# Performance work log

Measured on AMD Instinct MI355X. Metric: run time of the kernel, lower is better.

## Reference

```python
import jax, jax.numpy as jnp
import numpy as np
from jax import lax

EPS = 1e-5

def _conv(x, w, b, pad):
    y = lax.conv_general_dilated(x, w, (1, 1), [(pad, pad), (pad, pad)],
                                 dimension_numbers=('NCHW', 'OIHW', 'NCHW'))
    return y + b[None, :, None, None]

def _bn(x, g, b, m, v):
    # eval-mode BatchNorm2d with running stats
    scale = g * lax.rsqrt(v + EPS)
    return x * scale[None, :, None, None] + (b - m * scale)[None, :, None, None]

def setup_inputs() -> dict:
    key = jax.random.key(0)
    ks = jax.random.split(key, 16)
    B, C, H, W = 16, 64, 128, 128
    C2 = 2 * C
    d = {}
    d['x'] = jax.random.normal(ks[0], (B, C, H, W), jnp.float32)
    # fc1: Conv2d(C,C,3,p=1) + BN(C)
    d['fc1_w'] = jax.random.normal(ks[1], (C, C, 3, 3), jnp.float32) * 0.05
    d['fc1_b'] = jax.random.normal(ks[2], (C,), jnp.float32) * 0.05
    d['bn1_g'] = jnp.ones((C,), jnp.float32)
    d['bn1_b'] = jnp.zeros((C,), jnp.float32)
    d['bn1_m'] = jax.random.normal(ks[3], (C,), jnp.float32) * 0.05
    d['bn1_v'] = jax.random.uniform(ks[4], (C,), jnp.float32) * 0.5 + 0.5
    # graph_conv.nn: Conv2d(2C,2C,1) + BN(2C) + GELU
    d['gc_w'] = jax.random.normal(ks[5], (C2, C2, 1, 1), jnp.float32) * 0.05
    d['gc_b'] = jax.random.normal(ks[6], (C2,), jnp.float32) * 0.05
    d['bng_g'] = jnp.ones((C2,), jnp.float32)
    d['bng_b'] = jnp.zeros((C2,), jnp.float32)
    d['bng_m'] = jax.random.normal(ks[7], (C2,), jnp.float32) * 0.05
    d['bng_v'] = jax.random.uniform(ks[8], (C2,), jnp.float32) * 0.5 + 0.5
    # fc2: Conv2d(2C,C,3,p=1) + BN(C)
    d['fc2_w'] = jax.random.normal(ks[9], (C, C2, 3, 3), jnp.float32) * 0.05
    d['fc2_b'] = jax.random.normal(ks[10], (C,), jnp.float32) * 0.05
    d['bn2_g'] = jnp.ones((C,), jnp.float32)
    d['bn2_b'] = jnp.zeros((C,), jnp.float32)
    d['bn2_m'] = jax.random.normal(ks[11], (C,), jnp.float32) * 0.05
    d['bn2_v'] = jax.random.uniform(ks[12], (C,), jnp.float32) * 0.5 + 0.5
    return d

def reference(x, fc1_w, fc1_b, bn1_g, bn1_b, bn1_m, bn1_v,
              gc_w, gc_b, bng_g, bng_b, bng_m, bng_v,
              fc2_w, fc2_b, bn2_g, bn2_b, bn2_m, bn2_v):
    # fc1
    h = _bn(_conv(x, fc1_w, fc1_b, 1), bn1_g, bn1_b, bn1_m, bn1_v)
    # MRConv4dSP: strided self-attention over superpatch tokens
    sel = h[:, :, ::4, ::4]                          # [B,C,h4,w4]
    B, C, h4, w4 = sel.shape
    q = sel.reshape(B, C, h4 * w4).transpose(0, 2, 1)  # [B,N,C]
    scale = C ** (-0.5)
    att = jax.nn.softmax(jnp.einsum('bnc,bmc->bnm', q, q) * scale, axis=-1)
    o = jnp.einsum('bnm,bmc->bnc', att, q)           # [B,N,C]
    o = o.transpose(0, 2, 1).reshape(B, C, h4, w4)
    o = jnp.repeat(jnp.repeat(o, 4, axis=2), 4, axis=3)
    g = jnp.concatenate([h, o], axis=1)              # [B,2C,H,W]
    g = jax.nn.gelu(_bn(_conv(g, gc_w, gc_b, 0), bng_g, bng_b, bng_m, bng_v),
                    approximate=False)
    # fc2 + residual (drop_path=0 -> identity)
    y = _bn(_conv(g, fc2_w, fc2_b, 1), bn2_g, bn2_b, bn2_m, bn2_v)
    return y + x
```

## Files before the change

### kernel.cpp

```cpp
#include <hip/hip_runtime.h>
#include <math.h>

#define EPSV 1e-5f

typedef __bf16 bf16;
using bf16x8 = __attribute__((ext_vector_type(8))) __bf16;
using bf16x4 = __attribute__((ext_vector_type(4))) __bf16;
using bf16x2 = __attribute__((ext_vector_type(2))) __bf16;
using f32x4  = __attribute__((ext_vector_type(4))) float;

static __device__ __forceinline__ f32x4 mfma16(bf16x8 a, bf16x8 b, f32x4 c) {
    return __builtin_amdgcn_mfma_f32_16x16x32_bf16(a, b, c, 0, 0, 0);
}
static __device__ __forceinline__ f32x4 zero4() {
    f32x4 z = {0.f, 0.f, 0.f, 0.f};
    return z;
}

typedef __attribute__((address_space(1))) const char g_char_t;
typedef __attribute__((address_space(3))) char lds_char_t;
static __device__ __forceinline__ void gll16(const void* g, void* l) {
    __builtin_amdgcn_global_load_lds((g_char_t*)g, (lds_char_t*)l, 16, 0, 0);
}

static __device__ __forceinline__ float gelu_f(float v) {
    float z = fabsf(v) * 0.70710678118f;
    float t = __builtin_amdgcn_rcpf(1.f + 0.3275911f * z);
    float poly = t * (0.254829592f + t * (-0.284496736f + t * (1.421413741f +
                 t * (-1.453152027f + t * 1.061405429f))));
    float e = __expf(-z * z);
    float erfv = copysignf(1.f - poly * e, v);
    return 0.5f * v * (1.f + erfv);
}

template<int CIN>
__global__ __launch_bounds__(256) void prep_conv_w(const float* __restrict__ w,
                                                   bf16* __restrict__ wt)
{
    int t = blockIdx.x * 256 + threadIdx.x;
    if (t >= 64 * CIN) return;
    int cout = t / CIN, ci = t - cout * CIN;
    int cci = ci >> 5, lg = (ci >> 3) & 3, j = ci & 7;
    int mi = cout >> 4, lix = cout & 15;
#pragma unroll
    for (int kgt = 0; kgt < 9; ++kgt) {
        float v = w[(size_t)t * 9 + kgt];
        wt[((((size_t)kgt * (CIN >> 5) + cci) * 4 + mi) * 64 + lg * 16 + lix) * 8 + j]
            = (bf16)v;
    }
}

__global__ __launch_bounds__(256) void prep_1x1_w(const float* __restrict__ w,
                                                  bf16* __restrict__ wt)
{
    int t = blockIdx.x * 256 + threadIdx.x;
    int cout = t >> 7, ci = t & 127;
    int ks = ci >> 5, lg = (ci >> 3) & 3, j = ci & 7;
    wt[(((size_t)(ks * 4 + lg) * 128) + cout) * 8 + j] = (bf16)w[t];
}

__global__ __launch_bounds__(256) void cvt_x_nhwc(const float* __restrict__ x,
                                                  bf16* __restrict__ xb,
                                                  float* __restrict__ zb)
{
    __shared__ float t_lds[64 * 68];
    const int bx = blockIdx.x;
    const int b  = blockIdx.y;
    const int y  = bx >> 1, x0 = (bx & 1) * 64;
    const int tid = threadIdx.x;

    if (bx == 0 && b == 0 && tid < 64)
        ((float4*)zb)[tid] = make_float4(0.f, 0.f, 0.f, 0.f);

    for (int f = tid; f < 64 * 16; f += 256) {
        int c = f >> 4, xu = f & 15;
        float4 v = *(const float4*)&x[((size_t)(b * 64 + c) << 14) + (y << 7) + x0 + xu * 4];
        t_lds[(xu * 4 + 0) * 68 + c] = v.x;
        t_lds[(xu * 4 + 1) * 68 + c] = v.y;
        t_lds[(xu * 4 + 2) * 68 + c] = v.z;
        t_lds[(xu * 4 + 3) * 68 + c] = v.w;
    }
    __syncthreads();
    for (int f = tid; f < 64 * 8; f += 256) {
        int xx = f >> 3, cu = f & 7;
        const float* p = &t_lds[xx * 68 + cu * 8];
        bf16x8 v;
#pragma unroll
        for (int j = 0; j < 8; ++j) v[j] = (bf16)p[j];
        *(bf16x8*)&xb[((size_t)((b * 128 + y) * 128) + x0 + xx) * 64 + cu * 8] = v;
    }
}

template<int CIN, int OUTMODE>
__global__ __launch_bounds__(512) void conv3x3_mfma(
    const bf16* __restrict__ in, const bf16* __restrict__ wt,
    const float* __restrict__ bias,
    const float* __restrict__ bg, const float* __restrict__ bb,
    const float* __restrict__ bm, const float* __restrict__ bv,
    const bf16* __restrict__ resid, const bf16* __restrict__ zb,
    void* __restrict__ outp)
{
    constexpr int NC = CIN >> 5;
    __shared__ bf16 in_lds[672 * 32];
    __shared__ bf16 w_lds[36 * 512];

    const int wg = blockIdx.x;
    const int v  = (wg & 7) * 64 + (wg >> 3);
    const int tile = v & 31, b = v >> 5;
    const int x0 = (tile & 1) * 64;
    const int y0 = (tile >> 1) * 8;
    const int tid  = threadIdx.x;
    const int wid  = tid >> 6;
    const int lane = tid & 63;
    const int lix  = lane & 15, lg = lane >> 4;

    int goff[6]; bool gok[6];
#pragma unroll
    for (int i = 0; i < 6; ++i) {
        int chunk = wid + 8 * i;
        int f = chunk * 64 + lane;
        int pix = f >> 2, u = f & 3;
        int iy = pix / 66, ix = pix - iy * 66;
        int gy = y0 + iy - 1, gx = x0 + ix - 1;
        gok[i]  = (chunk < 42) && (pix < 660) &&
                  (unsigned)gy < 128u && (unsigned)gx < 128u;
        goff[i] = ((b * 128 + gy) * 128 + gx) * CIN + u * 8;
    }
    int rd[9];
#pragma unroll
    for (int kg = 0; kg < 3; ++kg)
#pragma unroll
        for (int t = 0; t < 3; ++t)
            rd[kg * 3 + t] = ((wid + kg) * 66 + lix + t) * 32 + lg * 8;

    f32x4 acc[4][4];
#pragma unroll
    for (int i = 0; i < 4; ++i)
#pragma unroll
        for (int j = 0; j < 4; ++j) acc[i][j] = zero4();

    auto issue_in = [&](int cci) {
#pragma unroll
        for (int i = 0; i < 6; ++i) {
            int chunk = wid + 8 * i;
            if (chunk < 42) {
                const void* src = gok[i] ? (const void*)(in + goff[i] + cci * 32)
                                         : (const void*)zb;
                gll16(src, (char*)in_lds + chunk * 1024);
            }
        }
    };
    auto issue_w = [&](int cci) {
#pragma unroll
        for (int i = 0; i < 5; ++i) {
            int chunk = wid + 8 * i;
            if (chunk < 36) {
                const bf16* src = wt + ((size_t)(chunk >> 2) * NC + cci) * 2048
                                     + (chunk & 3) * 512 + lane * 8;
                gll16(src, (char*)w_lds + chunk * 1024);
            }
        }
    };
    auto compute = [&]() {
#pragma unroll
        for (int kgt = 0; kgt < 9; ++kgt) {
            bf16x8 af[4];
#pragma unroll
            for (int mi = 0; mi < 4; ++mi)
                af[mi] = *(const bf16x8*)&w_lds[(kgt * 4 + mi) * 512 + lane * 8];
#pragma unroll
            for (int nj = 0; nj < 4; ++nj) {
                bf16x8 bfr = *(const bf16x8*)&in_lds[rd[kgt] + nj * 512];
#pragma unroll
                for (int mi = 0; mi < 4; ++mi)
                    acc[mi][nj] = mfma16(af[mi], bfr, acc[mi][nj]);
            }
        }
    };

    issue_in(0);
    issue_w(0);
#pragma unroll 1
    for (int c = 0; c < NC; ++c) {
        asm volatile("s_waitcnt vmcnt(0)" ::: "memory");
        __syncthreads();
        compute();
        if (c + 1 < NC) {
            __syncthreads();
            issue_in(c + 1);
            issue_w(c + 1);
        }
    }

    if (OUTMODE == 0) {
        bf16* out = (bf16*)outp;
        bf16* stg = in_lds;
#pragma unroll 1
        for (int p = 0; p < 2; ++p) {
            __syncthreads();
            if ((wid >> 2) == p) {
                int rl = wid & 3;
#pragma unroll
                for (int mi = 0; mi < 4; ++mi) {
                    float A[4], Bc[4];
#pragma unroll
                    for (int r = 0; r < 4; ++r) {
                        int c = mi * 16 + lg * 4 + r;
                        float s = bg[c] * rsqrtf(bv[c] + EPSV);
                        A[r]  = s;
                        Bc[r] = bias[c] * s + bb[c] - bm[c] * s;
                    }
#pragma unroll
                    for (int nj = 0; nj < 4; ++nj) {
                        int px = nj * 16 + lix;
                        bf16x4 vv;
#pragma unroll
                        for (int r = 0; r < 4; ++r)
                            vv[r] = (bf16)(acc[mi][nj][r] * A[r] + Bc[r]);
                        *(bf16x4*)&stg[(rl * 64 + px) * 68 + mi * 16 + lg * 4] = vv;
                    }
                }
            }
            __syncthreads();
#pragma unroll
            for (int k = 0; k < 4; ++k) {
                int idx = k * 512 + tid;
                int row = idx >> 9, rem = idx & 511;
                int px = rem >> 3, cu = rem & 7;
                bf16x8 vv = *(const bf16x8*)&stg[(row * 64 + px) * 68 + cu * 8];
                *(bf16x8*)&out[((size_t)((b * 128 + y0 + p * 4 + row) * 128)
                                + x0 + px) * 64 + cu * 8] = vv;
            }
        }
    } else {
        float* out = (float*)outp;
        const int gy = y0 + wid;
#pragma unroll
        for (int mi = 0; mi < 4; ++mi) {
            float A[4], Bc[4];
#pragma unroll
            for (int r = 0; r < 4; ++r) {
                int c = mi * 16 + lg * 4 + r;
                float s = bg[c] * rsqrtf(bv[c] + EPSV);
                A[r]  = s;
                Bc[r] = bias[c] * s + bb[c] - bm[c] * s;
            }
#pragma unroll
            for (int nj = 0; nj < 4; ++nj) {
                int px = x0 + nj * 16 + lix;
                bf16x4 rv = *(const bf16x4*)&resid[((size_t)((b * 128 + gy) * 128) + px) * 64
                                                   + mi * 16 + lg * 4];
#pragma unroll
                for (int r = 0; r < 4; ++r) {
                    int c = mi * 16 + lg * 4 + r;
                    size_t oi = ((size_t)(b * 64 + c) << 14) + (gy << 7) + px;
                    out[oi] = acc[mi][nj][r] * A[r] + Bc[r] + (float)rv[r];
                }
            }
        }
    }
}

__global__ __launch_bounds__(256) void gather_q(const bf16* __restrict__ h,
                                                bf16* __restrict__ q)
{
    int t = blockIdx.x * 256 + threadIdx.x;
    int cu = t & 7, n = (t >> 3) & 1023, b = t >> 13;
    int y = (n >> 5) << 2, x = (n & 31) << 2;
    bf16x8 v = *(const bf16x8*)&h[((size_t)((b * 128 + y) * 128 + x)) * 64 + cu * 8];
    *(bf16x8*)&q[((size_t)(b * 1024 + n)) * 64 + cu * 8] = v;
}

__global__ __launch_bounds__(256) void attn_fused(const bf16* __restrict__ q,
                                                  bf16* __restrict__ o)
{
    __shared__ bf16 qn[64 * 72];
    __shared__ bf16 kn[128 * 72];
    __shared__ bf16 vt[64 * 136];
    __shared__ bf16 pl[4][16 * 136];
    __shared__ __align__(16) float fac[4][16];
    const int n0 = blockIdx.x * 64, b = blockIdx.y;
    const int tid = threadIdx.x, w = tid >> 6, lane = tid & 63;
    const int lix = lane & 15, lg = lane >> 4;
    const bf16* qb = q + ((size_t)b << 16);

    for (int f = tid; f < 512; f += 256) {
        int row = f >> 3, cu = f & 7;
        *(bf16x8*)&qn[row * 72 + cu * 8] =
            *(const bf16x8*)&qb[(size_t)(n0 + row) * 64 + cu * 8];
    }

    float m_run = -3.0e38f, l_run = 0.f;
    f32x4 oacc[4];
#pragma unroll
    for (int ct = 0; ct < 4; ++ct) oacc[ct] = zero4();

    for (int mt = 0; mt < 1024; mt += 128) {
        __syncthreads();
        for (int f = tid; f < 1024; f += 256) {
            int row = f >> 3, cu = f & 7;
            *(bf16x8*)&kn[row * 72 + cu * 8] =
                *(const bf16x8*)&qb[(size_t)(mt + row) * 64 + cu * 8];
        }
        for (int f = tid; f < 512; f += 256) {
            int mp = f >> 3, cu = f & 7;
            int m = mp * 2;
            bf16x8 a = *(const bf16x8*)&qb[(size_t)(mt + m) * 64 + cu * 8];
            bf16x8 c = *(const bf16x8*)&qb[(size_t)(mt + m + 1) * 64 + cu * 8];
#pragma unroll
            for (int j = 0; j < 8; ++j) {
                bf16x2 pr = {a[j], c[j]};
                *(bf16x2*)&vt[(cu * 8 + j) * 136 + m] = pr;
            }
        }
        __syncthreads();

        bf16x8 bq0 = *(const bf16x8*)&qn[(w * 16 + lix) * 72 + lg * 8];
        bf16x8 bq1 = *(const bf16x8*)&qn[(w * 16 + lix) * 72 + 32 + lg * 8];

        f32x4 s[8];
#pragma unroll
        for (int t = 0; t < 8; ++t) {
            bf16x8 a0 = *(const bf16x8*)&kn[(t * 16 + lix) * 72 + lg * 8];
            bf16x8 a1 = *(const bf16x8*)&kn[(t * 16 + lix) * 72 + 32 + lg * 8];
            s[t] = mfma16(a0, bq0, zero4());
            s[t] = mfma16(a1, bq1, s[t]);
        }

        float mx = -3.0e38f;
#pragma unroll
        for (int t = 0; t < 8; ++t)
#pragma unroll
            for (int r = 0; r < 4; ++r) { s[t][r] *= 0.125f; mx = fmaxf(mx, s[t][r]); }
        mx = fmaxf(mx, __shfl_xor(mx, 16));
        mx = fmaxf(mx, __shfl_xor(mx, 32));
        float m_new = fmaxf(m_run, mx);
        float alpha = __expf(m_run - m_new);

        float psum = 0.f;
#pragma unroll
        for (int t = 0; t < 8; ++t) {
            float p0 = __expf(s[t][0] - m_new), p1 = __expf(s[t][1] - m_new);
            float p2 = __expf(s[t][2] - m_new), p3 = __expf(s[t][3] - m_new);
            psum += (p0 + p1) + (p2 + p3);
            bf16x2 v01 = {(bf16)p0, (bf16)p1};
            bf16x2 v23 = {(bf16)p2, (bf16)p3};
            *(bf16x2*)&pl[w][lix * 136 + t * 16 + lg * 4]     = v01;
            *(bf16x2*)&pl[w][lix * 136 + t * 16 + lg * 4 + 2] = v23;
        }
        psum += __shfl_xor(psum, 16);
        psum += __shfl_xor(psum, 32);
        l_run = l_run * alpha + psum;
        m_run = m_new;
        if (lg == 0) fac[w][lix] = alpha;

        float4 a4 = *(const float4*)&fac[w][lg * 4];
        float aa[4] = {a4.x, a4.y, a4.z, a4.w};
#pragma unroll
        for (int ct = 0; ct < 4; ++ct)
#pragma unroll
            for (int r = 0; r < 4; ++r) oacc[ct][r] *= aa[r];

#pragma unroll
        for (int kk = 0; kk < 4; ++kk) {
            bf16x8 pa = *(const bf16x8*)&pl[w][lix * 136 + kk * 32 + lg * 8];
#pragma unroll
            for (int ct = 0; ct < 4; ++ct) {
                bf16x8 bv = *(const bf16x8*)&vt[(ct * 16 + lix) * 136 + kk * 32 + lg * 8];
                oacc[ct] = mfma16(pa, bv, oacc[ct]);
            }
        }
    }

    if (lg == 0) fac[w][lix] = l_run;
    float4 l4 = *(const float4*)&fac[w][lg * 4];
    float ll[4] = {1.f / l4.x, 1.f / l4.y, 1.f / l4.z, 1.f / l4.w};
#pragma unroll
    for (int ct = 0; ct < 4; ++ct)
#pragma unroll
        for (int r = 0; r < 4; ++r) {
            int n = n0 + w * 16 + lg * 4 + r;
            int c = ct * 16 + lix;
            o[((size_t)(b * 1024 + n)) * 64 + c] = (bf16)(oacc[ct][r] * ll[r]);
        }
}

__global__ __launch_bounds__(256) void conv1x1_mfma(
    const bf16* __restrict__ h, const bf16* __restrict__ ov,
    const bf16* __restrict__ wt, const float* __restrict__ bias,
    const float* __restrict__ bg, const float* __restrict__ bb,
    const float* __restrict__ bm, const float* __restrict__ bv,
    bf16* __restrict__ g)
{
    __shared__ bf16 in1[128 * 136];
    const int y = blockIdx.x, b = blockIdx.y;
    const int tid = threadIdx.x;
    const int wid = tid >> 6, lane = tid & 63;
    const int lix = lane & 15, lg = lane >> 4;
    const int wm = wid >> 1, wn = wid & 1;

    for (int f = tid; f < 128 * 16; f += 256) {
        int px = f >> 4, cu = f & 15;
        bf16x8 v;
        if (cu < 8) {
            v = *(const bf16x8*)&h[((size_t)((b * 128 + y) * 128 + px)) * 64 + cu * 8];
        } else {
            int n = ((y >> 2) << 5) + (px >> 2);
            v = *(const bf16x8*)&ov[((size_t)(b * 1024 + n)) * 64 + (cu - 8) * 8];
        }
        *(bf16x8*)&in1[px * 136 + cu * 8] = v;
    }
    __syncthreads();

    f32x4 acc[4][4];
#pragma unroll
    for (int i = 0; i < 4; ++i)
#pragma unroll
        for (int j = 0; j < 4; ++j) acc[i][j] = zero4();

#pragma unroll
    for (int ks = 0; ks < 4; ++ks) {
        bf16x8 af[4], bfv[4];
#pragma unroll
        for (int mi = 0; mi < 4; ++mi)
            af[mi] = *(const bf16x8*)&wt[(((size_t)(ks * 4 + lg) * 128) + wm * 64 + mi * 16 + lix) * 8];
#pragma unroll
        for (int nj = 0; nj < 4; ++nj)
            bfv[nj] = *(const bf16x8*)&in1[(wn * 64 + nj * 16 + lix) * 136 + ks * 32 + lg * 8];
#pragma unroll
        for (int mi = 0; mi < 4; ++mi)
#pragma unroll
            for (int nj = 0; nj < 4; ++nj)
                acc[mi][nj] = mfma16(af[mi], bfv[nj], acc[mi][nj]);
    }

    __syncthreads();
    bf16* stg = in1;
#pragma unroll
    for (int mi = 0; mi < 4; ++mi) {
        float A[4], Bc[4];
#pragma unroll
        for (int r = 0; r < 4; ++r) {
            int c = wm * 64 + mi * 16 + lg * 4 + r;
            float s = bg[c] * rsqrtf(bv[c] + EPSV);
            A[r]  = s;
            Bc[r] = bias[c] * s + bb[c] - bm[c] * s;
        }
#pragma unroll
        for (int nj = 0; nj < 4; ++nj) {
            int px = wn * 64 + nj * 16 + lix;
            bf16x4 vv;
#pragma unroll
            for (int r = 0; r < 4; ++r)
                vv[r] = (bf16)gelu_f(acc[mi][nj][r] * A[r] + Bc[r]);
            *(bf16x4*)&stg[px * 132 + wm * 64 + mi * 16 + lg * 4] = vv;
        }
    }
    __syncthreads();
#pragma unroll
    for (int k = 0; k < 8; ++k) {
        int idx = k * 256 + tid;
        int px = idx >> 4, cu = idx & 15;
        bf16x8 v = *(const bf16x8*)&stg[px * 132 + cu * 8];
        *(bf16x8*)&g[((size_t)((b * 128 + y) * 128) + px) * 128 + cu * 8] = v;
    }
}

extern "C" void kernel_launch(void* const* d_in, const int* in_sizes, int n_in,
                              void* d_out, int out_size, void* d_ws, size_t ws_size,
                              hipStream_t stream)
{
    const float* x     = (const float*)d_in[0];
    const float* fc1_w = (const float*)d_in[1];
    const float* fc1_b = (const float*)d_in[2];
    const float* bn1_g = (const float*)d_in[3];
    const float* bn1_b = (const float*)d_in[4];
    const float* bn1_m = (const float*)d_in[5];
    const float* bn1_v = (const float*)d_in[6];
    const float* gc_w  = (const float*)d_in[7];
    const float* gc_b  = (const float*)d_in[8];
    const float* bng_g = (const float*)d_in[9];
    const float* bng_b = (const float*)d_in[10];
    const float* bng_m = (const float*)d_in[11];
    const float* bng_v = (const float*)d_in[12];
    const float* fc2_w = (const float*)d_in[13];
    const float* fc2_b = (const float*)d_in[14];
    const float* bn2_g = (const float*)d_in[15];
    const float* bn2_b = (const float*)d_in[16];
    const float* bn2_m = (const float*)d_in[17];
    const float* bn2_v = (const float*)d_in[18];

    char* wsb = (char*)d_ws;
    bf16* x_bf = (bf16*)wsb;
    bf16* h    = (bf16*)(wsb + 33554432);
    bf16* g    = (bf16*)(wsb + 67108864);
    bf16* q    = (bf16*)(wsb + 134217728);
    bf16* o    = (bf16*)(wsb + 136314880);
    bf16* wt1  = (bf16*)(wsb + 138412032);
    bf16* wt2  = (bf16*)(wsb + 138485760);
    bf16* wtg  = (bf16*)(wsb + 138633216);
    bf16* zb   = (bf16*)(wsb + 138665984);

    prep_conv_w<64><<<16, 256, 0, stream>>>(fc1_w, wt1);
    prep_conv_w<128><<<32, 256, 0, stream>>>(fc2_w, wt2);
    prep_1x1_w<<<64, 256, 0, stream>>>(gc_w, wtg);

    cvt_x_nhwc<<<dim3(256, 16), 256, 0, stream>>>(x, x_bf, (float*)zb);

    conv3x3_mfma<64, 0><<<512, 512, 0, stream>>>(
        x_bf, wt1, fc1_b, bn1_g, bn1_b, bn1_m, bn1_v, nullptr, zb, h);

    gather_q<<<512, 256, 0, stream>>>(h, q);

    attn_fused<<<dim3(16, 16), 256, 0, stream>>>(q, o);

    conv1x1_mfma<<<dim3(128, 16), 256, 0, stream>>>(
        h, o, wtg, gc_b, bng_g, bng_b, bng_m, bng_v, g);

    conv3x3_mfma<128, 1><<<512, 512, 0, stream>>>(
        g, wt2, fc2_b, bn2_g, bn2_b, bn2_m, bn2_v, x_bf, zb, (float*)d_out);
}
```

Measured before the change: 189.2 us.

## Double-buffer conv3x3 LDS tiles to overlap global loads with MFMA compute

The 3x3 conv kernel now keeps two LDS buffers for input and weight tiles. It issues the next channel chunk's global-to-LDS loads before computing the current chunk, using per-wave partial vmcnt waits so only the older loads must complete. The bf16 output staging is also collapsed from two half-passes into a single pass, made possible by the larger LDS. In exchange the kernel roughly doubles its LDS use, which may lower occupancy, and it relies on hand-tuned vmcnt counts that must match the exact number of loads each wave issues.

```diff
diff --git a/kernel.cpp b/kernel.cpp
--- a/kernel.cpp
+++ b/kernel.cpp
@@ -101,8 +101,8 @@
     void* __restrict__ outp)
 {
     constexpr int NC = CIN >> 5;
-    __shared__ bf16 in_lds[672 * 32];
-    __shared__ bf16 w_lds[36 * 512];
+    __shared__ bf16 in_lds[2][672 * 32];
+    __shared__ bf16 w_lds[2][36 * 512];
 
     const int wg = blockIdx.x;
     const int v  = (wg & 7) * 64 + (wg >> 3);
@@ -139,38 +139,38 @@
 #pragma unroll
         for (int j = 0; j < 4; ++j) acc[i][j] = zero4();
 
-    auto issue_in = [&](int cci) {
+    auto issue_in = [&](int cci, int buf) {
 #pragma unroll
         for (int i = 0; i < 6; ++i) {
             int chunk = wid + 8 * i;
             if (chunk < 42) {
                 const void* src = gok[i] ? (const void*)(in + goff[i] + cci * 32)
                                          : (const void*)zb;
-                gll16(src, (char*)in_lds + chunk * 1024);
+                gll16(src, (char*)&in_lds[buf][0] + chunk * 1024);
             }
         }
     };
-    auto issue_w = [&](int cci) {
+    auto issue_w = [&](int cci, int buf) {
 #pragma unroll
         for (int i = 0; i < 5; ++i) {
             int chunk = wid + 8 * i;
             if (chunk < 36) {
                 const bf16* src = wt + ((size_t)(chunk >> 2) * NC + cci) * 2048
                                      + (chunk & 3) * 512 + lane * 8;
-                gll16(src, (char*)w_lds + chunk * 1024);
+                gll16(src, (char*)&w_lds[buf][0] + chunk * 1024);
             }
         }
     };
-    auto compute = [&]() {
+    auto compute = [&](int buf) {
 #pragma unroll
         for (int kgt = 0; kgt < 9; ++kgt) {
             bf16x8 af[4];
 #pragma unroll
             for (int mi = 0; mi < 4; ++mi)
-                af[mi] = *(const bf16x8*)&w_lds[(kgt * 4 + mi) * 512 + lane * 8];
+                af[mi] = *(const bf16x8*)&w_lds[buf][(kgt * 4 + mi) * 512 + lane * 8];
 #pragma unroll
             for (int nj = 0; nj < 4; ++nj) {
-                bf16x8 bfr = *(const bf16x8*)&in_lds[rd[kgt] + nj * 512];
+                bf16x8 bfr = *(const bf16x8*)&in_lds[buf][rd[kgt] + nj * 512];
 #pragma unroll
                 for (int mi = 0; mi < 4; ++mi)
                     acc[mi][nj] = mfma16(af[mi], bfr, acc[mi][nj]);
@@ -178,59 +178,57 @@
         }
     };
 
-    issue_in(0);
-    issue_w(0);
+    issue_in(0, 0);
+    issue_w(0, 0);
 #pragma unroll 1
     for (int c = 0; c < NC; ++c) {
-        asm volatile("s_waitcnt vmcnt(0)" ::: "memory");
-        __syncthreads();
-        compute();
         if (c + 1 < NC) {
-            __syncthreads();
-            issue_in(c + 1);
-            issue_w(c + 1);
-        }
+            issue_in(c + 1, (c + 1) & 1);
+            issue_w(c + 1, (c + 1) & 1);
+            if (wid < 2)      asm volatile("s_waitcnt vmcnt(11)" ::: "memory");
+            else if (wid < 4) asm volatile("s_waitcnt vmcnt(10)" ::: "memory");
+            else              asm volatile("s_waitcnt vmcnt(9)"  ::: "memory");
+        } else {
+            asm volatile("s_waitcnt vmcnt(0)" ::: "memory");
+        }
+        __builtin_amdgcn_s_barrier();
+        __builtin_amdgcn_sched_barrier(0);
+        compute(c & 1);
+        __builtin_amdgcn_s_barrier();
     }
 
     if (OUTMODE == 0) {
         bf16* out = (bf16*)outp;
-        bf16* stg = in_lds;
-#pragma unroll 1
-        for (int p = 0; p < 2; ++p) {
-            __syncthreads();
-            if ((wid >> 2) == p) {
-                int rl = wid & 3;
-#pragma unroll
-                for (int mi = 0; mi < 4; ++mi) {
-                    float A[4], Bc[4];
-#pragma unroll
-                    for (int r = 0; r < 4; ++r) {
-                        int c = mi * 16 + lg * 4 + r;
-                        float s = bg[c] * rsqrtf(bv[c] + EPSV);
-                        A[r]  = s;
-                        Bc[r] = bias[c] * s + bb[c] - bm[c] * s;
-                    }
-#pragma unroll
-                    for (int nj = 0; nj < 4; ++nj) {
-                        int px = nj * 16 + lix;
-                        bf16x4 vv;
-#pragma unroll
-                        for (int r = 0; r < 4; ++r)
-                            vv[r] = (bf16)(acc[mi][nj][r] * A[r] + Bc[r]);
-                        *(bf16x4*)&stg[(rl * 64 + px) * 68 + mi * 16 + lg * 4] = vv;
-                    }
-                }
-            }
-            __syncthreads();
-#pragma unroll
-            for (int k = 0; k < 4; ++k) {
-                int idx = k * 512 + tid;
-                int row = idx >> 9, rem = idx & 511;
-                int px = rem >> 3, cu = rem & 7;
-                bf16x8 vv = *(const bf16x8*)&stg[(row * 64 + px) * 68 + cu * 8];
-                *(bf16x8*)&out[((size_t)((b * 128 + y0 + p * 4 + row) * 128)
-                                + x0 + px) * 64 + cu * 8] = vv;
-            }
+        bf16* stg = &in_lds[0][0];
+#pragma unroll
+        for (int mi = 0; mi < 4; ++mi) {
+            float A[4], Bc[4];
+#pragma unroll
+            for (int r = 0; r < 4; ++r) {
+                int c = mi * 16 + lg * 4 + r;
+                float s = bg[c] * rsqrtf(bv[c] + EPSV);
+                A[r]  = s;
+                Bc[r] = bias[c] * s + bb[c] - bm[c] * s;
+            }
+#pragma unroll
+            for (int nj = 0; nj < 4; ++nj) {
+                int px = nj * 16 + lix;
+                bf16x4 vv;
+#pragma unroll
+                for (int r = 0; r < 4; ++r)
+                    vv[r] = (bf16)(acc[mi][nj][r] * A[r] + Bc[r]);
+                *(bf16x4*)&stg[(wid * 64 + px) * 68 + mi * 16 + lg * 4] = vv;
+            }
+        }
+        __syncthreads();
+#pragma unroll
+        for (int k = 0; k < 8; ++k) {
+            int idx = k * 512 + tid;
+            int row = idx >> 9, rem = idx & 511;
+            int px = rem >> 3, cu = rem & 7;
+            bf16x8 vv = *(const bf16x8*)&stg[(row * 64 + px) * 68 + cu * 8];
+            *(bf16x8*)&out[((size_t)((b * 128 + y0 + row) * 128)
+                            + x0 + px) * 64 + cu * 8] = vv;
         }
     } else {
         float* out = (float*)outp;
```

Measured after the change: 186.7 us. Within noise of the previous version (-1.4%).
